# Kernel optimization log

Hardware: AMD Instinct MI355X
Metric: run time of the kernel (lower is better)

Reference implementation:

```python
import jax, jax.numpy as jnp
import numpy as np
import math

B, L, DIM = 2, 2048, 1024
HEADS = 16
DH = DIM // HEADS  # 64
M_IALSH = 2
U_IALSH = 0.75
NEG = -1e4  # additive mask value for non-matching hash buckets


def setup_inputs() -> dict:
    key = jax.random.key(0)
    k0, k1, k2, k3 = jax.random.split(key, 4)
    return {
        "hidden_states": jax.random.normal(k0, (B, L, DIM), jnp.float32),
        "qk_w": jax.random.normal(k1, (DIM, DIM), jnp.float32) * 0.02,
        "qk_b": jnp.zeros((DIM,), jnp.float32),
        "v_w": jax.random.normal(k2, (DIM, DIM), jnp.float32) * 0.02,
        "v_b": jnp.zeros((DIM,), jnp.float32),
        "hash_a": jax.random.normal(k3, (DH + M_IALSH,), jnp.float32),
    }


def _ialsh_mask(qkh, hash_a):
    # qkh: (b, h, l, dh). IALSH (Improved Asymmetric LSH for MIPS):
    # keys scaled so max norm per (b,h) is U; P(x)=[x, 1/2-||x||^2, 1/2-||x||^4]
    # queries unit-normalized;        Q(x)=[x/||x||, 0, 0]
    norms = jnp.linalg.norm(qkh, axis=-1, keepdims=True)          # (b,h,l,1)
    max_norm = jnp.max(norms, axis=2, keepdims=True)              # (b,h,1,1)
    xk = qkh * (U_IALSH / jnp.maximum(max_norm, 1e-12))
    nk2 = jnp.sum(xk * xk, axis=-1, keepdims=True)                # ||x||^2
    P = jnp.concatenate([xk, 0.5 - nk2, 0.5 - nk2 * nk2], axis=-1)
    q_unit = qkh / jnp.maximum(norms, 1e-12)
    zeros = jnp.zeros_like(nk2)
    Q = jnp.concatenate([q_unit, zeros, zeros], axis=-1)
    hq = (Q @ hash_a) >= 0.0                                      # (b,h,l) sign hash
    hk = (P @ hash_a) >= 0.0
    same = hq[..., :, None] == hk[..., None, :]                   # (b,h,l,l)
    return jnp.where(same, 0.0, NEG).astype(qkh.dtype)


def reference(hidden_states, qk_w, qk_b, v_w, v_b, hash_a):
    b, l, d = hidden_states.shape
    qk = hidden_states @ qk_w.T + qk_b                            # shared Q/K projection
    v = hidden_states @ v_w.T + v_b

    def split(x):  # (b,l,d) -> (b,h,l,dh)
        return x.reshape(b, l, HEADS, DH).transpose(0, 2, 1, 3)

    qkh, vh = split(qk), split(v)
    scores = jnp.einsum('bhqd,bhkd->bhqk', qkh, qkh) / math.sqrt(DH)
    scores = scores + _ialsh_mask(qkh, hash_a)
    probs = jax.nn.softmax(scores, axis=-1)  # dropout = identity (eval mode)
    ctx = jnp.einsum('bhqk,bhkd->bhqd', probs, vh)
    return ctx.transpose(0, 2, 1, 3).reshape(b, l, d)
```

## Files before the change

### kernel.cpp

```cpp
#include <hip/hip_runtime.h>

typedef unsigned short u16;
typedef unsigned char  u8;
typedef unsigned int   u32;
typedef unsigned long long u64;

typedef short bf16x8 __attribute__((ext_vector_type(8)));
typedef float f32x4  __attribute__((ext_vector_type(4)));
typedef float f32x16 __attribute__((ext_vector_type(16)));

#define DEV __device__ __forceinline__

#if __has_builtin(__builtin_amdgcn_exp2f)
#define EXP2(x) __builtin_amdgcn_exp2f(x)
#else
#define EXP2(x) exp2f(x)
#endif

DEV u16 f2bf(float x) {
  u32 u = __builtin_bit_cast(u32, x);
  u32 r = (u + 0x7fffu + ((u >> 16) & 1u)) >> 16;
  return (u16)r;
}
DEV float bf2f(u16 h) {
  u32 u = ((u32)h) << 16;
  return __builtin_bit_cast(float, u);
}
DEV f32x4 mfma16(bf16x8 a, bf16x8 b, f32x4 c) {
  return __builtin_amdgcn_mfma_f32_16x16x32_bf16(a, b, c, 0, 0, 0);
}
DEV f32x16 mfma32(bf16x8 a, bf16x8 b, f32x16 c) {
  return __builtin_amdgcn_mfma_f32_32x32x16_bf16(a, b, c, 0, 0, 0);
}
DEV u32 cvtpk(float lo, float hi) {
  u32 r;
  asm("v_cvt_pk_bf16_f32 %0, %1, %2" : "=v"(r) : "v"(lo), "v"(hi));
  return r;
}
DEV void pswap(u32& x, u32& y) {
  asm("v_permlane32_swap_b32 %0, %1" : "+v"(x), "+v"(y));
}
DEV bf16x8 mkfrag(u32 w0, u32 w1, u32 w2, u32 w3) {
  union { u32 w[4]; bf16x8 v; } u;
  u.w[0] = w0; u.w[1] = w1; u.w[2] = w2; u.w[3] = w3;
  return u.v;
}

#define GLDS(gptr, lptr)                                                  \
  __builtin_amdgcn_global_load_lds(                                       \
      (const __attribute__((address_space(1))) void*)(gptr),              \
      (__attribute__((address_space(3))) void*)(lptr), 16, 0, 0)

__global__ __launch_bounds__(256) void split3_kernel(
    const float* __restrict__ hid, const float* __restrict__ wq,
    const float* __restrict__ wv,
    u16* __restrict__ hHi, u16* __restrict__ hLo,
    u16* __restrict__ wqHi, u16* __restrict__ wqLo, u16* __restrict__ wvHi) {
  const int NH4 = 1048576, NW4 = 262144;
  int i = blockIdx.x * 256 + threadIdx.x;
  if (i < NH4) {
    float4 v = ((const float4*)hid)[i];
    ushort4 h, l;
    h.x = f2bf(v.x); l.x = f2bf(v.x - bf2f(h.x));
    h.y = f2bf(v.y); l.y = f2bf(v.y - bf2f(h.y));
    h.z = f2bf(v.z); l.z = f2bf(v.z - bf2f(h.z));
    h.w = f2bf(v.w); l.w = f2bf(v.w - bf2f(h.w));
    ((ushort4*)hHi)[i] = h;
    ((ushort4*)hLo)[i] = l;
  } else if (i < NH4 + NW4) {
    int j = i - NH4;
    float4 v = ((const float4*)wq)[j];
    ushort4 h, l;
    h.x = f2bf(v.x); l.x = f2bf(v.x - bf2f(h.x));
    h.y = f2bf(v.y); l.y = f2bf(v.y - bf2f(h.y));
    h.z = f2bf(v.z); l.z = f2bf(v.z - bf2f(h.z));
    h.w = f2bf(v.w); l.w = f2bf(v.w - bf2f(h.w));
    ((ushort4*)wqHi)[j] = h;
    ((ushort4*)wqLo)[j] = l;
  } else {
    int j = i - NH4 - NW4;
    float4 v = ((const float4*)wv)[j];
    ushort4 h;
    h.x = f2bf(v.x); h.y = f2bf(v.y); h.z = f2bf(v.z); h.w = f2bf(v.w);
    ((ushort4*)wvHi)[j] = h;
  }
}

__global__ __launch_bounds__(256) void ca_kernel(
    const float* __restrict__ W, const float* __restrict__ ha, double* __restrict__ ca) {
  int idx = blockIdx.x * 256 + threadIdx.x;
  int h = idx >> 10, k = idx & 1023;
  double s = 0.0;
#pragma unroll 8
  for (int j = 0; j < 64; ++j)
    s += (double)W[(size_t)(h * 64 + j) * 1024 + k] * (double)ha[j];
  ca[idx] = s;
}

__global__ __launch_bounds__(256) void d_kernel(
    const float* __restrict__ hid, const double* __restrict__ ca, float* __restrict__ dq) {
  const int row0 = blockIdx.x * 8 + (threadIdx.x >> 6) * 2;
  const int lane = threadIdx.x & 63;
  double a0[16], a1[16];
#pragma unroll
  for (int h = 0; h < 16; ++h) { a0[h] = 0.0; a1[h] = 0.0; }
  const float* hp = hid + (size_t)row0 * 1024;
  for (int k = lane; k < 1024; k += 64) {
    const double h0 = (double)hp[k];
    const double h1 = (double)hp[k + 1024];
#pragma unroll
    for (int h = 0; h < 16; ++h) {
      const double c = ca[h * 1024 + k];
      a0[h] += h0 * c;
      a1[h] += h1 * c;
    }
  }
#pragma unroll
  for (int h = 0; h < 16; ++h) {
    double v0 = a0[h], v1 = a1[h];
#pragma unroll
    for (int off = 32; off; off >>= 1) {
      v0 += __shfl_xor(v0, off, 64);
      v1 += __shfl_xor(v1, off, 64);
    }
    if (lane == 0) {
      const int b0 = row0 >> 11, l0 = row0 & 2047;
      dq[(size_t)(b0 * 16 + h) * 2048 + l0] = (float)v0;
      const int r1 = row0 + 1;
      dq[(size_t)((r1 >> 11) * 16 + h) * 2048 + (r1 & 2047)] = (float)v1;
    }
  }
}

__global__ __launch_bounds__(256, 2) void gemm_fused(
    const u16* __restrict__ hHi, const u16* __restrict__ hLo,
    const u16* __restrict__ wqHi, const u16* __restrict__ wqLo,
    const u16* __restrict__ wvHi,
    const float* __restrict__ qk_b, const float* __restrict__ v_b,
    u16* __restrict__ qkB, u16* __restrict__ vT, float* __restrict__ n2A) {
  constexpr int K = 1024;
  __shared__ u16 S[2][16384];
  const int tid = threadIdx.x, wave = tid >> 6, lane = tid & 63;
  const int quad = lane >> 4, lm = lane & 15;
  const int wr = wave >> 1, wc = wave & 1;
  const int m0 = blockIdx.x * 64, n0 = blockIdx.y * 128;
  const int ch = lane & 3, rA = lane >> 2;

  auto stage = [&](int kt, int buf) {
    const int k0 = kt * 32;
    const int rowA = wave * 16 + rA;
    GLDS(hHi + (size_t)(m0 + rowA) * K + k0 + ch * 8, &S[buf][0 + wave * 512]);
    GLDS(hLo + (size_t)(m0 + rowA) * K + k0 + ch * 8, &S[buf][2048 + wave * 512]);
#pragma unroll
    for (int it = 0; it < 2; ++it) {
      const int rb = wave * 2 + it;
      const int row = rb * 16 + rA;
      GLDS(wqHi + (size_t)(n0 + row) * K + k0 + ch * 8, &S[buf][4096 + rb * 512]);
      GLDS(wqLo + (size_t)(n0 + row) * K + k0 + ch * 8, &S[buf][8192 + rb * 512]);
      GLDS(wvHi + (size_t)(n0 + row) * K + k0 + ch * 8, &S[buf][12288 + rb * 512]);
    }
  };

  f32x4 aq[2][4], av[4][2];
#pragma unroll
  for (int i = 0; i < 2; ++i)
#pragma unroll
    for (int j = 0; j < 4; ++j) aq[i][j] = {0.f, 0.f, 0.f, 0.f};
#pragma unroll
  for (int i = 0; i < 4; ++i)
#pragma unroll
    for (int j = 0; j < 2; ++j) av[i][j] = {0.f, 0.f, 0.f, 0.f};

  stage(0, 0);
  __syncthreads();

  for (int kt = 0; kt < 32; ++kt) {
    const int cur = kt & 1;
    if (kt < 31) stage(kt + 1, cur ^ 1);

    bf16x8 a_h[2], a_l[2], b_h[4], b_l[4], w_h[4];
#pragma unroll
    for (int i = 0; i < 2; ++i) {
      a_h[i] = *(const bf16x8*)&S[cur][(wr * 32 + i * 16 + lm) * 32 + quad * 8];
      a_l[i] = *(const bf16x8*)&S[cur][2048 + (wr * 32 + i * 16 + lm) * 32 + quad * 8];
    }
#pragma unroll
    for (int j = 0; j < 4; ++j) {
      b_h[j] = *(const bf16x8*)&S[cur][4096 + (wc * 64 + j * 16 + lm) * 32 + quad * 8];
      b_l[j] = *(const bf16x8*)&S[cur][8192 + (wc * 64 + j * 16 + lm) * 32 + quad * 8];
      w_h[j] = *(const bf16x8*)&S[cur][12288 + (wc * 64 + j * 16 + lm) * 32 + quad * 8];
    }
#pragma unroll
    for (int i = 0; i < 2; ++i)
#pragma unroll
      for (int j = 0; j < 4; ++j) {
        aq[i][j] = mfma16(a_h[i], b_h[j], aq[i][j]);
        aq[i][j] = mfma16(a_h[i], b_l[j], aq[i][j]);
        aq[i][j] = mfma16(a_l[i], b_h[j], aq[i][j]);
      }
#pragma unroll
    for (int iv = 0; iv < 4; ++iv)
#pragma unroll
      for (int jv = 0; jv < 2; ++jv)
        av[iv][jv] = mfma16(w_h[iv], a_h[jv], av[iv][jv]);

    __syncthreads();
  }

  const int hidx = blockIdx.y * 2 + wc;
#pragma unroll
  for (int i = 0; i < 2; ++i) {
    float nn[4] = {0.f, 0.f, 0.f, 0.f};
#pragma unroll
    for (int j = 0; j < 4; ++j) {
      const int col = n0 + wc * 64 + j * 16 + lm;
      const float bv = qk_b[col];
#pragma unroll
      for (int r = 0; r < 4; ++r) {
        const int row = m0 + wr * 32 + i * 16 + quad * 4 + r;
        const float val = aq[i][j][r] + bv;
        qkB[(size_t)row * 1024 + col] = f2bf(val);
        nn[r] += val * val;
      }
    }
#pragma unroll
    for (int r = 0; r < 4; ++r)
#pragma unroll
      for (int off = 1; off < 16; off <<= 1) nn[r] += __shfl_xor(nn[r], off, 64);
    if (lm == 0) {
      const int row = m0 + wr * 32 + i * 16 + quad * 4;
      const int b = row >> 11, l = row & 2047;
      *(float4*)&n2A[(size_t)(b * 16 + hidx) * 2048 + l] =
          make_float4(nn[0], nn[1], nn[2], nn[3]);
    }
  }
#pragma unroll
  for (int iv = 0; iv < 4; ++iv)
#pragma unroll
    for (int r = 0; r < 4; ++r) {
      const int vcol = n0 + wc * 64 + iv * 16 + quad * 4 + r;
      const float bv = v_b[vcol];
#pragma unroll
      for (int jv = 0; jv < 2; ++jv) {
        const int tok = m0 + wr * 32 + jv * 16 + lm;
        vT[(size_t)vcol * 4096 + tok] = f2bf(av[iv][jv][r] + bv);
      }
    }
}

__global__ __launch_bounds__(256) void bits_kernel(
    const float* __restrict__ n2A, const float* __restrict__ dq,
    const float* __restrict__ ha, u8* __restrict__ hqA, u64* __restrict__ hkM) {
  const int bh = blockIdx.x;
  const int tid = threadIdx.x;
  const int wave = tid >> 6, lane = tid & 63;
  __shared__ float red[4];
  const float* n2p = n2A + (size_t)bh * 2048;
  float4 v0 = ((const float4*)n2p)[tid];
  float4 v1 = ((const float4*)n2p)[tid + 256];
  float lmax = fmaxf(fmaxf(fmaxf(v0.x, v0.y), fmaxf(v0.z, v0.w)),
                     fmaxf(fmaxf(v1.x, v1.y), fmaxf(v1.z, v1.w)));
#pragma unroll
  for (int off = 1; off < 64; off <<= 1) lmax = fmaxf(lmax, __shfl_xor(lmax, off, 64));
  if (lane == 0) red[wave] = lmax;
  __syncthreads();
  const float maxn2 = fmaxf(fmaxf(red[0], red[1]), fmaxf(red[2], red[3]));
  const float s = 0.75f / fmaxf(sqrtf(maxn2), 1e-12f);
  const float a64 = ha[64], a65 = ha[65];
#pragma unroll
  for (int it = 0; it < 8; ++it) {
    const int l = it * 256 + tid;
    const float dv = dq[(size_t)bh * 2048 + l];
    const float n2 = n2p[l];
    const float nk2 = s * s * n2;
    const float hkdot = s * dv + (0.5f - nk2) * a64 + (0.5f - nk2 * nk2) * a65;
    hqA[(size_t)bh * 2048 + l] = (dv >= 0.f) ? 1 : 0;
    const u64 m = __ballot(hkdot >= 0.f);
    if (lane == 0) hkM[(size_t)bh * 32 + it * 4 + wave] = m;
  }
}

__global__ __launch_bounds__(256, 2) void attn_kernel(
    const u16* __restrict__ qkb, const u16* __restrict__ vT,
    const u8* __restrict__ hqA, const u64* __restrict__ hkM,
    float* __restrict__ out) {
  __shared__ u16 Ks[2][4096];
  __shared__ u16 Vs[2][4096];

  const int id = blockIdx.x;
  const int bh = id & 31, qt = id >> 5;
  const int b = bh >> 4, h = bh & 15;
  const int tid = threadIdx.x, wave = tid >> 6, lane = tid & 63;
  const int col = lane & 31;
  const int hf = lane >> 5;
  const int ch7 = col & 7;
  const int r8 = lane >> 3, ch = lane & 7;
  const int q0 = qt * 128;
  const int token = q0 + wave * 32 + col;

  const u16* qbase = qkb + (size_t)b * 2048 * 1024 + h * 64;
  const u16* vtb = vT + (size_t)h * 64 * 4096 + b * 2048;
  const u64* hkp = hkM + (size_t)bh * 32;

  bf16x8 aQ[4];
#pragma unroll
  for (int c = 0; c < 4; ++c)
    aQ[c] = *(const bf16x8*)(qbase + (size_t)token * 1024 + c * 16 + hf * 8);
  const u32 hqx = hqA[(size_t)bh * 2048 + token] ? 0xFFFFFFFFu : 0u;

  const int srow = wave * 16;
  auto stage = [&](int kt, int buf) {
#pragma unroll
    for (int i = 0; i < 2; ++i) {
      const int row = srow + i * 8 + r8;
      const int sw = (ch ^ (row & 7)) * 8;
      GLDS(qbase + (size_t)(kt * 64 + row) * 1024 + sw, &Ks[buf][(srow + i * 8) * 64]);
      GLDS(vtb + (size_t)row * 4096 + kt * 64 + sw, &Vs[buf][(srow + i * 8) * 64]);
    }
  };

  f32x16 acc[2];
#pragma unroll
  for (int d = 0; d < 2; ++d)
#pragma unroll
    for (int r = 0; r < 16; ++r) acc[d][r] = 0.f;
  float accL = 0.f;

  const float SCL = 0.18033688f;
  const float M0 = -4.3280854f;

  u64 mk = hkp[0];
  stage(0, 0);
  __syncthreads();

  for (int kt = 0; kt < 32; ++kt) {
    const int cur = kt & 1;
    if (kt < 31) stage(kt + 1, cur ^ 1);
    const u64 mk_next = (kt < 31) ? hkp[kt + 1] : 0ull;

    const u64 msh = mk >> (hf * 4);
    u32 mw[2];
    mw[0] = (u32)msh;
    mw[1] = (u32)(msh >> 32);

#pragma unroll
    for (int kb = 0; kb < 2; ++kb) {
      const u32 hw = mw[kb] ^ hqx;
      f32x16 cs;
#pragma unroll
      for (int r = 0; r < 16; ++r) cs[r] = 0.f;
      __builtin_amdgcn_s_setprio(1);
#pragma unroll
      for (int c = 0; c < 4; ++c) {
        const bf16x8 aK = *(const bf16x8*)
            &Ks[cur][(kb * 32 + col) * 64 + (((c * 2 + hf) ^ ch7) * 8)];
        cs = mfma32(aK, aQ[c], cs);
      }
      __builtin_amdgcn_s_setprio(0);

      float pv[16];
#pragma unroll
      for (int r = 0; r < 16; ++r) {
        const int pos = (r & 3) + 8 * (r >> 2);
        float p = EXP2(__builtin_fmaf(cs[r], SCL, M0));
        p = ((hw >> pos) & 1u) ? 0.f : p;
        accL += p;
        pv[r] = p;
      }
      u32 pk[8];
#pragma unroll
      for (int i = 0; i < 8; ++i) pk[i] = cvtpk(pv[2 * i], pv[2 * i + 1]);
      pswap(pk[0], pk[2]);
      pswap(pk[1], pk[3]);
      pswap(pk[4], pk[6]);
      pswap(pk[5], pk[7]);
      const bf16x8 fr0 = mkfrag(pk[0], pk[1], pk[2], pk[3]);
      const bf16x8 fr1 = mkfrag(pk[4], pk[5], pk[6], pk[7]);

      __builtin_amdgcn_s_setprio(1);
#pragma unroll
      for (int db = 0; db < 2; ++db) {
        const bf16x8 aV0 = *(const bf16x8*)
            &Vs[cur][(db * 32 + col) * 64 + ((((kb * 2 + 0) * 2 + hf) ^ ch7) * 8)];
        acc[db] = mfma32(aV0, fr0, acc[db]);
        const bf16x8 aV1 = *(const bf16x8*)
            &Vs[cur][(db * 32 + col) * 64 + ((((kb * 2 + 1) * 2 + hf) ^ ch7) * 8)];
        acc[db] = mfma32(aV1, fr1, acc[db]);
      }
      __builtin_amdgcn_s_setprio(0);
    }

    mk = mk_next;
    __syncthreads();
  }

  accL += __shfl_xor(accL, 32);
  const float inv = 1.0f / accL;
  float* op = out + (size_t)(b * 2048 + token) * 1024 + h * 64 + hf * 4;
#pragma unroll
  for (int db = 0; db < 2; ++db)
#pragma unroll
    for (int g = 0; g < 4; ++g) {
      float4 v4 = make_float4(acc[db][g * 4 + 0] * inv, acc[db][g * 4 + 1] * inv,
                              acc[db][g * 4 + 2] * inv, acc[db][g * 4 + 3] * inv);
      *(float4*)(op + db * 32 + g * 8) = v4;
    }
}

extern "C" void kernel_launch(void* const* d_in, const int* in_sizes, int n_in,
                              void* d_out, int out_size, void* d_ws, size_t ws_size,
                              hipStream_t stream) {
  const float* hidden = (const float*)d_in[0];
  const float* qk_w   = (const float*)d_in[1];
  const float* qk_b   = (const float*)d_in[2];
  const float* v_w    = (const float*)d_in[3];
  const float* v_b    = (const float*)d_in[4];
  const float* hash_a = (const float*)d_in[5];
  float* out = (float*)d_out;

  char* base = (char*)d_ws;
  size_t off = 0;
  auto take = [&](size_t bytes) -> char* {
    char* r = base + off;
    off += (bytes + 255) & ~(size_t)255;
    return r;
  };
  const size_t NH = 4194304;
  const size_t NW = 1048576;
  u16* hHi  = (u16*)take(NH * 2);
  u16* hLo  = (u16*)take(NH * 2);
  u16* wqHi = (u16*)take(NW * 2);
  u16* wqLo = (u16*)take(NW * 2);
  u16* wvHi = (u16*)take(NW * 2);
  u16* qkB  = (u16*)take(NH * 2);
  u16* vT   = (u16*)take(NH * 2);
  double* ca = (double*)take(16 * 1024 * 8);
  float* dq  = (float*)take(65536 * 4);
  float* n2A = (float*)take(65536 * 4);
  u8* hqA = (u8*)take(65536);
  u64* hkM = (u64*)take(32 * 32 * 8);

  hipLaunchKernelGGL(split3_kernel, dim3(6144), dim3(256), 0, stream,
                     hidden, qk_w, v_w, hHi, hLo, wqHi, wqLo, wvHi);
  hipLaunchKernelGGL(ca_kernel, dim3(64), dim3(256), 0, stream, qk_w, hash_a, ca);
  hipLaunchKernelGGL(d_kernel, dim3(512), dim3(256), 0, stream, hidden, ca, dq);
  hipLaunchKernelGGL(gemm_fused, dim3(64, 8), dim3(256), 0, stream,
                     hHi, hLo, wqHi, wqLo, wvHi, qk_b, v_b, qkB, vT, n2A);
  hipLaunchKernelGGL(bits_kernel, dim3(32), dim3(256), 0, stream, n2A, dq, hash_a, hqA, hkM);
  hipLaunchKernelGGL(attn_kernel, dim3(512), dim3(256), 0, stream, qkB, vT, hqA, hkM, out);
}
```

Before: 220.1 us.

## Split attention key range across two blocks and add a combine kernel

Each attention block now processes half of the key tiles, doubling the grid. Unnormalized partial outputs and row sums go to the output and to reused workspace buffers, and a new combine kernel sums them and normalizes. This relies on the fixed softmax offset, so no max rescaling is needed. It aims to raise parallelism and tail balance at the cost of extra global traffic for partials and one more launch.

```diff
diff --git a/kernel.cpp b/kernel.cpp
--- a/kernel.cpp
+++ b/kernel.cpp
@@ -283,12 +283,13 @@
 __global__ __launch_bounds__(256, 2) void attn_kernel(
     const u16* __restrict__ qkb, const u16* __restrict__ vT,
     const u8* __restrict__ hqA, const u64* __restrict__ hkM,
-    float* __restrict__ out) {
+    float* __restrict__ out, float* __restrict__ pO1,
+    float* __restrict__ pL0, float* __restrict__ pL1) {
   __shared__ u16 Ks[2][4096];
   __shared__ u16 Vs[2][4096];
 
   const int id = blockIdx.x;
-  const int bh = id & 31, qt = id >> 5;
+  const int bh = id & 31, qt = (id >> 5) & 15, kz = id >> 9;
   const int b = bh >> 4, h = bh & 15;
   const int tid = threadIdx.x, wave = tid >> 6, lane = tid & 63;
   const int col = lane & 31;
@@ -297,6 +298,7 @@
   const int r8 = lane >> 3, ch = lane & 7;
   const int q0 = qt * 128;
   const int token = q0 + wave * 32 + col;
+  const int kts = kz * 16, kte = kts + 16;
 
   const u16* qbase = qkb + (size_t)b * 2048 * 1024 + h * 64;
   const u16* vtb = vT + (size_t)h * 64 * 4096 + b * 2048;
@@ -329,14 +331,14 @@
   const float SCL = 0.18033688f;
   const float M0 = -4.3280854f;
 
-  u64 mk = hkp[0];
-  stage(0, 0);
+  u64 mk = hkp[kts];
+  stage(kts, 0);
   __syncthreads();
 
-  for (int kt = 0; kt < 32; ++kt) {
+  for (int kt = kts; kt < kte; ++kt) {
     const int cur = kt & 1;
-    if (kt < 31) stage(kt + 1, cur ^ 1);
-    const u64 mk_next = (kt < 31) ? hkp[kt + 1] : 0ull;
+    if (kt + 1 < kte) stage(kt + 1, cur ^ 1);
+    const u64 mk_next = (kt + 1 < kte) ? hkp[kt + 1] : 0ull;
 
     const u64 msh = mk >> (hf * 4);
     u32 mw[2];
@@ -395,16 +397,33 @@
   }
 
   accL += __shfl_xor(accL, 32);
-  const float inv = 1.0f / accL;
-  float* op = out + (size_t)(b * 2048 + token) * 1024 + h * 64 + hf * 4;
+  float* obase = kz ? pO1 : out;
+  float* lbase = kz ? pL1 : pL0;
+  if (hf == 0) lbase[(size_t)bh * 2048 + token] = accL;
+  float* op = obase + (size_t)(b * 2048 + token) * 1024 + h * 64 + hf * 4;
 #pragma unroll
   for (int db = 0; db < 2; ++db)
 #pragma unroll
     for (int g = 0; g < 4; ++g) {
-      float4 v4 = make_float4(acc[db][g * 4 + 0] * inv, acc[db][g * 4 + 1] * inv,
-                              acc[db][g * 4 + 2] * inv, acc[db][g * 4 + 3] * inv);
+      float4 v4 = make_float4(acc[db][g * 4 + 0], acc[db][g * 4 + 1],
+                              acc[db][g * 4 + 2], acc[db][g * 4 + 3]);
       *(float4*)(op + db * 32 + g * 8) = v4;
     }
+}
+
+__global__ __launch_bounds__(256) void combine_kernel(
+    const float* __restrict__ pO1, const float* __restrict__ pL0,
+    const float* __restrict__ pL1, float* __restrict__ out) {
+  const int j = blockIdx.x * 256 + threadIdx.x;
+  const int row = j >> 8;
+  const int h = (j & 255) >> 4;
+  const int b = row >> 11, l = row & 2047;
+  const size_t li = (size_t)(b * 16 + h) * 2048 + l;
+  const float inv = 1.0f / (pL0[li] + pL1[li]);
+  const float4 a = ((const float4*)out)[j];
+  const float4 c = ((const float4*)pO1)[j];
+  ((float4*)out)[j] = make_float4((a.x + c.x) * inv, (a.y + c.y) * inv,
+                                  (a.z + c.z) * inv, (a.w + c.w) * inv);
 }
 
 extern "C" void kernel_launch(void* const* d_in, const int* in_sizes, int n_in,
@@ -440,6 +459,10 @@
   u8* hqA = (u8*)take(65536);
   u64* hkM = (u64*)take(32 * 32 * 8);
 
+  float* pO1 = (float*)hHi;
+  float* pL0 = (float*)wqHi;
+  float* pL1 = pL0 + 65536;
+
   hipLaunchKernelGGL(split3_kernel, dim3(6144), dim3(256), 0, stream,
                      hidden, qk_w, v_w, hHi, hLo, wqHi, wqLo, wvHi);
   hipLaunchKernelGGL(ca_kernel, dim3(64), dim3(256), 0, stream, qk_w, hash_a, ca);
@@ -447,5 +470,8 @@
   hipLaunchKernelGGL(gemm_fused, dim3(64, 8), dim3(256), 0, stream,
                      hHi, hLo, wqHi, wqLo, wvHi, qk_b, v_b, qkB, vT, n2A);
   hipLaunchKernelGGL(bits_kernel, dim3(32), dim3(256), 0, stream, n2A, dq, hash_a, hqA, hkM);
-  hipLaunchKernelGGL(attn_kernel, dim3(512), dim3(256), 0, stream, qkB, vT, hqA, hkM, out);
-}
+  hipLaunchKernelGGL(attn_kernel, dim3(1024), dim3(256), 0, stream,
+                     qkB, vT, hqA, hkM, out, pO1, pL0, pL1);
+  hipLaunchKernelGGL(combine_kernel, dim3(4096), dim3(256), 0, stream,
+                     pO1, pL0, pL1, out);
+}
```

Result: slower. 224.7 us (+2.1%).
